# Kernel optimization log

Hardware: AMD Instinct MI355X
Metric: run time of the kernel (lower is better)

## Reference

```python
import jax, jax.numpy as jnp
import numpy as np

N_NODES = 50000
N_EDGES = 800000
D = 96
LN_EPS = 1e-5


def setup_inputs() -> dict:
    key = jax.random.key(0)
    ks = jax.random.split(key, 4)
    x = jax.random.normal(ks[0], (N_NODES, D), dtype=jnp.float32)
    edge_index = jax.random.randint(ks[1], (2, N_EDGES), 0, N_NODES, dtype=jnp.int64)
    scale = 1.0 / np.sqrt(D)
    W0 = jax.random.normal(ks[2], (D, D), dtype=jnp.float32) * scale
    W1 = jax.random.normal(ks[3], (D, D), dtype=jnp.float32) * scale
    b0 = jnp.zeros((D,), jnp.float32)
    b1 = jnp.zeros((D,), jnp.float32)
    g0 = jnp.ones((D,), jnp.float32)
    g1 = jnp.ones((D,), jnp.float32)
    be0 = jnp.zeros((D,), jnp.float32)
    be1 = jnp.zeros((D,), jnp.float32)
    return {"x": x, "edge_index": edge_index, "W0": W0, "b0": b0, "g0": g0,
            "be0": be0, "W1": W1, "b1": b1, "g1": g1, "be1": be1}


def _layer(h, src, dst, norm, n_nodes, W, b, g, be):
    # GCNConv: h' = scatter_add(norm * (h W)[src]) + b  (self-loops included in src/dst)
    h = h @ W                                  # [N, out]
    msg = h[src] * norm[:, None]               # [E+N, out] gather (memory-bound)
    h = jax.ops.segment_sum(msg, dst, num_segments=n_nodes) + b
    h = jnp.tanh(h)
    mu = jnp.mean(h, axis=-1, keepdims=True)
    var = jnp.mean(jnp.square(h - mu), axis=-1, keepdims=True)
    h = (h - mu) * jax.lax.rsqrt(var + LN_EPS)
    return h * g + be


def reference(x, edge_index, W0, b0, g0, be0, W1, b1, g1, be1):
    n = x.shape[0]
    loops = jnp.arange(n, dtype=edge_index.dtype)
    src = jnp.concatenate([edge_index[0], loops])  # add self-loops (PyG default)
    dst = jnp.concatenate([edge_index[1], loops])
    deg = jax.ops.segment_sum(jnp.ones(src.shape, x.dtype), dst, num_segments=n)
    dis = jax.lax.rsqrt(deg)                       # deg >= 1 due to self-loops
    norm = dis[src] * dis[dst]                     # symmetric normalization
    h = _layer(x, src, dst, norm, n, W0, b0, g0, be0)
    h = _layer(h, src, dst, norm, n, W1, b1, g1, be1)
    return h  # dropout is identity in eval mode
```

## Files before the change

kernel.cpp:

```cpp
#include <hip/hip_runtime.h>
#include <hip/hip_bf16.h>
#include <type_traits>

#define D 96
#define LN_EPS 1e-5f
#define CHUNK 1024
#define BCAP 8192
#define BCAPP (BCAP + 1792)

typedef unsigned short ushort_t;
typedef __attribute__((ext_vector_type(8))) short short8;
typedef __attribute__((ext_vector_type(4))) float f32x4;

__device__ __forceinline__ ushort_t f2bf(float f) {
    unsigned u = __float_as_uint(f);
    u += 0x7FFF + ((u >> 16) & 1);
    return (ushort_t)(u >> 16);
}
__device__ __forceinline__ float blo(unsigned v) {
    return __uint_as_float(v << 16);
}
__device__ __forceinline__ float bhi(unsigned v) {
    return __uint_as_float(v & 0xffff0000u);
}

__global__ __launch_bounds__(256) void k_init(const unsigned* __restrict__ w,
                                              int* __restrict__ flag,
                                              int* __restrict__ gcur,
                                              unsigned* __restrict__ hsA,
                                              unsigned* __restrict__ hsB, int N,
                                              int nbuk,
                                              const float* __restrict__ W0,
                                              const float* __restrict__ W1,
                                              ushort_t* __restrict__ Wt0,
                                              ushort_t* __restrict__ Wt1) {
    int t = threadIdx.x;
    if (blockIdx.x == 0) {
        __shared__ int anynz;
        if (t == 0) anynz = 0;
        __syncthreads();
        if ((t & 1) && w[t] != 0) anynz = 1;
        if (t < nbuk) gcur[t] = t * BCAP;
        if (t < 32) hsA[(size_t)N * 32 + t] = 0;
        if (t < 16) hsB[(size_t)N * 16 + t] = 0;
        __syncthreads();
        if (t == 0) *flag = (anynz == 0) ? 1 : 0;
    } else {
        int idx = (blockIdx.x - 1) * 256 + t;
        int sel = idx / 9216, i = idx % 9216;
        int c = i / 96, k = i % 96;
        const float* W = sel ? W1 : W0;
        ushort_t* Wt = sel ? Wt1 : Wt0;
        Wt[c * 96 + k] = f2bf(W[k * 96 + c]);
    }
}

__device__ __forceinline__ int load_idx(const void* eb, int is64, long long pos) {
    if (is64) return (int)((const long long*)eb)[pos];
    return ((const int*)eb)[pos];
}

__global__ __launch_bounds__(256) void k_bfill(const void* __restrict__ eb,
                                               const int* __restrict__ flag,
                                               int* __restrict__ gcur,
                                               unsigned* __restrict__ part, int E) {
    __shared__ int hist[2][256];
    __shared__ int cur[2][256];
    int t = threadIdx.x;
    int half = t >> 7;
    hist[0][t] = 0; hist[1][t] = 0;
    __syncthreads();
    int is64 = *flag;
    long long base = (long long)blockIdx.x * CHUNK;
    int sv[CHUNK / 256];
    int dv[CHUNK / 256];
    #pragma unroll
    for (int i = 0; i < CHUNK / 256; ++i) {
        long long e = base + t + (long long)i * 256;
        if (e < E) {
            sv[i] = load_idx(eb, is64, e);
            dv[i] = load_idx(eb, is64, (long long)E + e);
            atomicAdd(&hist[half][dv[i] >> 8], 1);
        } else dv[i] = -1;
    }
    __syncthreads();
    int h0 = hist[0][t], tot = h0 + hist[1][t];
    int b0 = 0;
    if (tot > 0) b0 = atomicAdd(&gcur[t], tot);
    cur[0][t] = b0;
    cur[1][t] = b0 + h0;
    __syncthreads();
    #pragma unroll
    for (int i = 0; i < CHUNK / 256; ++i) {
        if (dv[i] >= 0) {
            int b = dv[i] >> 8;
            int pos = atomicAdd(&cur[half][b], 1);
            part[pos] = ((unsigned)sv[i] << 8) | (unsigned)(dv[i] & 255);
        }
    }
}

__global__ __launch_bounds__(256) void k_build(const unsigned* __restrict__ part,
                                               const int* __restrict__ gcur,
                                               int2* __restrict__ rr,
                                               int* __restrict__ csr_src,
                                               float* __restrict__ dis,
                                               int N) {
    __shared__ int bins[2][256];
    __shared__ int cur[2][256];
    __shared__ int sh[256];
    int t = threadIdx.x;
    int b = blockIdx.x;
    int half = t >> 7;
    int beg = b * BCAP, end = gcur[b];
    bins[0][t] = 0; bins[1][t] = 0;
    __syncthreads();
    for (int i = beg + t; i < end; i += 256)
        atomicAdd(&bins[half][part[i] & 255u], 1);
    __syncthreads();
    int d0 = bins[0][t];
    int deg = d0 + bins[1][t];
    int pdeg = (deg + 7) & ~7;
    sh[t] = pdeg;
    __syncthreads();
    for (int off = 1; off < 256; off <<= 1) {
        int x = (t >= off) ? sh[t - off] : 0;
        __syncthreads();
        sh[t] += x;
        __syncthreads();
    }
    int mybeg = b * BCAPP + (sh[t] - pdeg);
    int node = b * 256 + t;
    if (node < N) {
        rr[node] = make_int2(mybeg, mybeg + pdeg);
        dis[node] = rsqrtf((float)(deg + 1));
    }
    cur[0][t] = mybeg;
    cur[1][t] = mybeg + d0;
    __syncthreads();
    for (int i = beg + t; i < end; i += 256) {
        unsigned p = part[i];
        int pos = atomicAdd(&cur[half][p & 255u], 1);
        csr_src[pos] = (int)(p >> 8);
    }
    for (int k = deg; k < pdeg; ++k) csr_src[mybeg + k] = N;
}

template<typename T>
__global__ __launch_bounds__(256) void k_gemm_mfma(const T* __restrict__ A0,
                                                   const T* __restrict__ A1,
                                                   const ushort_t* __restrict__ Wt,
                                                   const float* __restrict__ dis,
                                                   ushort_t* __restrict__ HsA,
                                                   ushort_t* __restrict__ HsB, int N) {
    __shared__ ushort_t As[64][104];
    __shared__ ushort_t Bs[96][104];
    int t = threadIdx.x;
    int row0 = blockIdx.x * 64;

    if constexpr (std::is_same<T, float>::value) {
        const float4* X4 = (const float4*)A0;
        #pragma unroll
        for (int i = 0; i < 6; ++i) {
            int idx = t + i * 256;
            int r = idx / 24, c4 = idx % 24;
            float4 v = make_float4(0.f, 0.f, 0.f, 0.f);
            if (row0 + r < N) v = X4[(size_t)(row0 + r) * 24 + c4];
            ushort4 o;
            o.x = f2bf(v.x); o.y = f2bf(v.y); o.z = f2bf(v.z); o.w = f2bf(v.w);
            *(ushort4*)&As[r][c4 * 4] = o;
        }
    } else {
        #pragma unroll
        for (int i = 0; i < 3; ++i) {
            int idx = t + i * 256;
            int r = idx / 12, c8 = idx % 12;
            short8 v = {0, 0, 0, 0, 0, 0, 0, 0};
            if (row0 + r < N) {
                if (c8 < 8) v = *(const short8*)(A0 + (size_t)(row0 + r) * 64 + c8 * 8);
                else        v = *(const short8*)(A1 + (size_t)(row0 + r) * 32 + (c8 - 8) * 8);
            }
            *(short8*)&As[r][c8 * 8] = v;
        }
    }
    #pragma unroll
    for (int i = 0; i < 5; ++i) {
        int idx = t + i * 256;
        if (idx < 1152) {
            int r = idx / 12, c8 = idx % 12;
            *(short8*)&Bs[r][c8 * 8] = *(const short8*)(Wt + r * 96 + c8 * 8);
        }
    }
    __syncthreads();

    int w = t >> 6, l = t & 63;
    int lr = l & 15, lq = l >> 4;
    f32x4 acc[6];
    #pragma unroll
    for (int c = 0; c < 6; ++c) acc[c] = (f32x4){0.f, 0.f, 0.f, 0.f};

    #pragma unroll
    for (int q = 0; q < 3; ++q) {
        short8 af = *(const short8*)&As[w * 16 + lr][q * 32 + lq * 8];
        #pragma unroll
        for (int c = 0; c < 6; ++c) {
            short8 bf = *(const short8*)&Bs[c * 16 + lr][q * 32 + lq * 8];
            acc[c] = __builtin_amdgcn_mfma_f32_16x16x32_bf16(af, bf, acc[c], 0, 0, 0);
        }
    }

    int rbase = row0 + w * 16 + lq * 4;
    #pragma unroll
    for (int r = 0; r < 4; ++r) {
        int gr = rbase + r;
        if (gr < N) {
            float dr = dis[gr];
            ushort_t* oA = HsA + (size_t)gr * 64 + lr;
            ushort_t* oB = HsB + (size_t)gr * 32 + lr;
            #pragma unroll
            for (int c = 0; c < 4; ++c) oA[c * 16] = f2bf(dr * acc[c][r]);
            #pragma unroll
            for (int c = 4; c < 6; ++c) oB[(c - 4) * 16] = f2bf(dr * acc[c][r]);
        }
    }
}

template<bool BF16OUT>
__global__ __launch_bounds__(256) void k_agg_ln(const unsigned* __restrict__ hA32,
                                                const unsigned* __restrict__ hB32,
                                                const int2* __restrict__ rr,
                                                const int* __restrict__ csr_src,
                                                const float* __restrict__ dis,
                                                const float* __restrict__ b,
                                                const float* __restrict__ g,
                                                const float* __restrict__ be,
                                                void* __restrict__ outA,
                                                void* __restrict__ outB, int N) {
    int node = blockIdx.x * 8 + (threadIdx.x >> 5);
    int lane = threadIdx.x & 31;
    if (node >= N) return;

    float a0, a1, c0 = 0.f, c1 = 0.f;
    {
        unsigned v = hA32[(size_t)node * 32 + lane];
        a0 = blo(v); a1 = bhi(v);
        if (lane < 16) {
            unsigned u = hB32[(size_t)node * 16 + lane];
            c0 = blo(u); c1 = bhi(u);
        }
    }

    int2 r = rr[node];
    int beg = r.x, end = r.y;
    int lsel = lane >> 4;
    int lb = lane & 15;
    for (int cb = beg; cb < end; cb += 32) {
        int m = min(32, end - cb);
        int e = cb + lane;
        int sreg = (e < end) ? csr_src[e] : (int)N;
        for (int j = 0; j < m; j += 8) {
            int s0 = __shfl(sreg, j, 32);
            int s1 = __shfl(sreg, j + 1, 32);
            int s2 = __shfl(sreg, j + 2, 32);
            int s3 = __shfl(sreg, j + 3, 32);
            int s4 = __shfl(sreg, j + 4, 32);
            int s5 = __shfl(sreg, j + 5, 32);
            int s6 = __shfl(sreg, j + 6, 32);
            int s7 = __shfl(sreg, j + 7, 32);
            int p0 = __shfl(sreg, j + lsel, 32);
            int p1 = __shfl(sreg, j + 2 + lsel, 32);
            int p2 = __shfl(sreg, j + 4 + lsel, 32);
            int p3 = __shfl(sreg, j + 6 + lsel, 32);
            unsigned v0 = hA32[s0 * 32 + lane];
            unsigned v1 = hA32[s1 * 32 + lane];
            unsigned v2 = hA32[s2 * 32 + lane];
            unsigned v3 = hA32[s3 * 32 + lane];
            unsigned v4 = hA32[s4 * 32 + lane];
            unsigned v5 = hA32[s5 * 32 + lane];
            unsigned v6 = hA32[s6 * 32 + lane];
            unsigned v7 = hA32[s7 * 32 + lane];
            unsigned w0 = hB32[p0 * 16 + lb];
            unsigned w1 = hB32[p1 * 16 + lb];
            unsigned w2 = hB32[p2 * 16 + lb];
            unsigned w3 = hB32[p3 * 16 + lb];
            a0 += blo(v0) + blo(v1) + blo(v2) + blo(v3)
                + blo(v4) + blo(v5) + blo(v6) + blo(v7);
            a1 += bhi(v0) + bhi(v1) + bhi(v2) + bhi(v3)
                + bhi(v4) + bhi(v5) + bhi(v6) + bhi(v7);
            c0 += blo(w0) + blo(w1) + blo(w2) + blo(w3);
            c1 += bhi(w0) + bhi(w1) + bhi(w2) + bhi(w3);
        }
    }

    c0 += __shfl_xor(c0, 16, 32);
    c1 += __shfl_xor(c1, 16, 32);

    float dn = dis[node];
    float2 b01 = ((const float2*)b)[lane];
    a0 = tanhf(fmaf(dn, a0, b01.x));
    a1 = tanhf(fmaf(dn, a1, b01.y));
    float s1 = a0 + a1;
    float s2 = a0 * a0 + a1 * a1;
    float a2 = 0.f, a3 = 0.f;
    if (lane < 16) {
        float2 b23 = ((const float2*)b)[32 + lane];
        a2 = tanhf(fmaf(dn, c0, b23.x));
        a3 = tanhf(fmaf(dn, c1, b23.y));
        s1 += a2 + a3;
        s2 += a2 * a2 + a3 * a3;
    }
    #pragma unroll
    for (int off = 16; off >= 1; off >>= 1) {
        s1 += __shfl_xor(s1, off, 32);
        s2 += __shfl_xor(s2, off, 32);
    }
    float mu = s1 * (1.f / 96.f);
    float var = s2 * (1.f / 96.f) - mu * mu;
    float inv = rsqrtf(var + LN_EPS);

    float2 g01 = ((const float2*)g)[lane];
    float2 e01 = ((const float2*)be)[lane];
    float r0 = (a0 - mu) * inv * g01.x + e01.x;
    float r1 = (a1 - mu) * inv * g01.y + e01.y;
    if (BF16OUT) {
        ((unsigned*)outA)[(size_t)node * 32 + lane] =
            ((unsigned)f2bf(r1) << 16) | (unsigned)f2bf(r0);
        if (lane < 16) {
            float2 g23 = ((const float2*)g)[32 + lane];
            float2 e23 = ((const float2*)be)[32 + lane];
            float r2 = (a2 - mu) * inv * g23.x + e23.x;
            float r3 = (a3 - mu) * inv * g23.y + e23.y;
            ((unsigned*)outB)[(size_t)node * 16 + lane] =
                ((unsigned)f2bf(r3) << 16) | (unsigned)f2bf(r2);
        }
    } else {
        float2* o2 = (float2*)((float*)outA + (size_t)node * D);
        o2[lane] = make_float2(r0, r1);
        if (lane < 16) {
            float2 g23 = ((const float2*)g)[32 + lane];
            float2 e23 = ((const float2*)be)[32 + lane];
            o2[32 + lane] = make_float2((a2 - mu) * inv * g23.x + e23.x,
                                        (a3 - mu) * inv * g23.y + e23.y);
        }
    }
}

extern "C" void kernel_launch(void* const* d_in, const int* in_sizes, int n_in,
                              void* d_out, int out_size, void* d_ws, size_t ws_size,
                              hipStream_t stream) {
    const float* x  = (const float*)d_in[0];
    const void*  eb = d_in[1];
    const float* W0 = (const float*)d_in[2];
    const float* b0 = (const float*)d_in[3];
    const float* g0 = (const float*)d_in[4];
    const float* be0 = (const float*)d_in[5];
    const float* W1 = (const float*)d_in[6];
    const float* b1 = (const float*)d_in[7];
    const float* g1 = (const float*)d_in[8];
    const float* be1 = (const float*)d_in[9];

    const int N = in_sizes[0] / D;
    const int E = in_sizes[1] / 2;
    const int NBUK = (N + 255) >> 8;
    const int NBLK = (E + CHUNK - 1) / CHUNK;

    auto al = [](size_t v) { return (v + 255) & ~(size_t)255; };
    char* w = (char*)d_ws;
    size_t off = 0;
    int* flag = (int*)(w + off);          off = al(off + 4);
    int* gcur = (int*)(w + off);          off = al(off + 256 * 4);
    int2* rr = (int2*)(w + off);          off = al(off + (size_t)N * 8);
    float* dis = (float*)(w + off);       off = al(off + (size_t)N * 4);
    int* csr_src = (int*)(w + off);       off = al(off + ((size_t)NBUK * BCAPP + 64) * 4);
    unsigned* part = (unsigned*)(w + off); off = al(off + ((size_t)NBUK * BCAP + BCAP) * 4);
    unsigned* hsA = (unsigned*)(w + off); off = al(off + ((size_t)N + 1) * 128);
    unsigned* hsB = (unsigned*)(w + off); off = al(off + ((size_t)N + 1) * 64);
    ushort_t* h1A = (ushort_t*)(w + off); off = al(off + (size_t)N * 128);
    ushort_t* h1B = (ushort_t*)(w + off); off = al(off + (size_t)N * 64);
    ushort_t* Wt0 = (ushort_t*)(w + off); off = al(off + 9216 * 2);
    ushort_t* Wt1 = (ushort_t*)(w + off); off = al(off + 9216 * 2);
    float* outf = (float*)d_out;

    const int nbG = (N + 63) / 64;
    const int nbA = (N + 7) / 8;

    k_init<<<73, 256, 0, stream>>>((const unsigned*)eb, flag, gcur, hsA, hsB, N,
                                   NBUK, W0, W1, Wt0, Wt1);
    k_bfill<<<NBLK, 256, 0, stream>>>(eb, flag, gcur, part, E);
    k_build<<<NBUK, 256, 0, stream>>>(part, gcur, rr, csr_src, dis, N);

    k_gemm_mfma<float><<<nbG, 256, 0, stream>>>(x, (const float*)nullptr, Wt0, dis,
                                                (ushort_t*)hsA, (ushort_t*)hsB, N);
    k_agg_ln<true><<<nbA, 256, 0, stream>>>(hsA, hsB, rr, csr_src, dis,
                                            b0, g0, be0, (void*)h1A, (void*)h1B, N);
    k_gemm_mfma<ushort_t><<<nbG, 256, 0, stream>>>(h1A, h1B, Wt1, dis,
                                                   (ushort_t*)hsA, (ushort_t*)hsB, N);
    k_agg_ln<false><<<nbA, 256, 0, stream>>>(hsA, hsB, rr, csr_src, dis,
                                             b1, g1, be1, (void*)outf, nullptr, N);
}
```

Before: 120.4 us.

## Fuse layer-0 GEMM with edge bucketing and relocate degree scaling

The first-layer MFMA GEMM and the edge bucket-fill now run as interleaved block roles of one launch, so the dense work overlaps the atomic-heavy partitioning. Because the GEMM then runs before degrees are known, k_build rescales the projected rows by dis in place. The second layer's dis scaling moves into the layer-1 aggregation output, which is valid because row scaling commutes with the matmul. The weight transpose is folded into each GEMM's shared-memory load, dropping the separate transpose blocks and buffers. The cost is an extra read-modify-write pass over the projected features and a second bf16 rounding of those values.

```diff
diff --git a/kernel.cpp b/kernel.cpp
--- a/kernel.cpp
+++ b/kernel.cpp
@@ -1,6 +1,5 @@
 #include <hip/hip_runtime.h>
 #include <hip/hip_bf16.h>
-#include <type_traits>
 
 #define D 96
 #define LN_EPS 1e-5f
@@ -23,36 +22,26 @@
 __device__ __forceinline__ float bhi(unsigned v) {
     return __uint_as_float(v & 0xffff0000u);
 }
+__device__ __forceinline__ unsigned pack2(float lo, float hi) {
+    return ((unsigned)f2bf(hi) << 16) | (unsigned)f2bf(lo);
+}
 
 __global__ __launch_bounds__(256) void k_init(const unsigned* __restrict__ w,
                                               int* __restrict__ flag,
                                               int* __restrict__ gcur,
                                               unsigned* __restrict__ hsA,
-                                              unsigned* __restrict__ hsB, int N,
-                                              int nbuk,
-                                              const float* __restrict__ W0,
-                                              const float* __restrict__ W1,
-                                              ushort_t* __restrict__ Wt0,
-                                              ushort_t* __restrict__ Wt1) {
+                                              unsigned* __restrict__ hsB,
+                                              int N, int nbuk) {
+    __shared__ int anynz;
     int t = threadIdx.x;
-    if (blockIdx.x == 0) {
-        __shared__ int anynz;
-        if (t == 0) anynz = 0;
-        __syncthreads();
-        if ((t & 1) && w[t] != 0) anynz = 1;
-        if (t < nbuk) gcur[t] = t * BCAP;
-        if (t < 32) hsA[(size_t)N * 32 + t] = 0;
-        if (t < 16) hsB[(size_t)N * 16 + t] = 0;
-        __syncthreads();
-        if (t == 0) *flag = (anynz == 0) ? 1 : 0;
-    } else {
-        int idx = (blockIdx.x - 1) * 256 + t;
-        int sel = idx / 9216, i = idx % 9216;
-        int c = i / 96, k = i % 96;
-        const float* W = sel ? W1 : W0;
-        ushort_t* Wt = sel ? Wt1 : Wt0;
-        Wt[c * 96 + k] = f2bf(W[k * 96 + c]);
-    }
+    if (t == 0) anynz = 0;
+    __syncthreads();
+    if ((t & 1) && w[t] != 0) anynz = 1;
+    if (t < nbuk) gcur[t] = t * BCAP;
+    if (t < 32) hsA[(size_t)N * 32 + t] = 0;
+    if (t < 16) hsB[(size_t)N * 16 + t] = 0;
+    __syncthreads();
+    if (t == 0) *flag = (anynz == 0) ? 1 : 0;
 }
 
 __device__ __forceinline__ int load_idx(const void* eb, int is64, long long pos) {
@@ -60,42 +49,117 @@
     return ((const int*)eb)[pos];
 }
 
-__global__ __launch_bounds__(256) void k_bfill(const void* __restrict__ eb,
-                                               const int* __restrict__ flag,
-                                               int* __restrict__ gcur,
-                                               unsigned* __restrict__ part, int E) {
-    __shared__ int hist[2][256];
-    __shared__ int cur[2][256];
+union Smem1 {
+    struct { ushort_t As[64][104]; ushort_t Bs[96][104]; } g;
+    struct { int hist[2][256]; int cur[2][256]; } b;
+};
+
+__global__ __launch_bounds__(256) void k_fused1(const float* __restrict__ X,
+                                                const float* __restrict__ W0,
+                                                ushort_t* __restrict__ HsA,
+                                                ushort_t* __restrict__ HsB,
+                                                int N, int nbG,
+                                                const void* __restrict__ eb,
+                                                const int* __restrict__ flag,
+                                                int* __restrict__ gcur,
+                                                unsigned* __restrict__ part, int E,
+                                                int NBLK) {
+    __shared__ Smem1 u;
     int t = threadIdx.x;
-    int half = t >> 7;
-    hist[0][t] = 0; hist[1][t] = 0;
-    __syncthreads();
-    int is64 = *flag;
-    long long base = (long long)blockIdx.x * CHUNK;
-    int sv[CHUNK / 256];
-    int dv[CHUNK / 256];
-    #pragma unroll
-    for (int i = 0; i < CHUNK / 256; ++i) {
-        long long e = base + t + (long long)i * 256;
-        if (e < E) {
-            sv[i] = load_idx(eb, is64, e);
-            dv[i] = load_idx(eb, is64, (long long)E + e);
-            atomicAdd(&hist[half][dv[i] >> 8], 1);
-        } else dv[i] = -1;
-    }
-    __syncthreads();
-    int h0 = hist[0][t], tot = h0 + hist[1][t];
-    int b0 = 0;
-    if (tot > 0) b0 = atomicAdd(&gcur[t], tot);
-    cur[0][t] = b0;
-    cur[1][t] = b0 + h0;
-    __syncthreads();
-    #pragma unroll
-    for (int i = 0; i < CHUNK / 256; ++i) {
-        if (dv[i] >= 0) {
-            int b = dv[i] >> 8;
-            int pos = atomicAdd(&cur[half][b], 1);
-            part[pos] = ((unsigned)sv[i] << 8) | (unsigned)(dv[i] & 255);
+    int bid = blockIdx.x;
+    int mn = min(nbG, NBLK);
+    int isG, idx;
+    if (bid < 2 * mn) { isG = !(bid & 1); idx = bid >> 1; }
+    else {
+        int r = bid - 2 * mn;
+        if (nbG > NBLK) { isG = 1; idx = mn + r; }
+        else            { isG = 0; idx = mn + r; }
+    }
+
+    if (isG) {
+        int row0 = idx * 64;
+        const float4* X4 = (const float4*)X;
+        #pragma unroll
+        for (int i = 0; i < 6; ++i) {
+            int id2 = t + i * 256;
+            int r = id2 / 24, c4 = id2 % 24;
+            float4 v = make_float4(0.f, 0.f, 0.f, 0.f);
+            if (row0 + r < N) v = X4[(size_t)(row0 + r) * 24 + c4];
+            ushort4 o;
+            o.x = f2bf(v.x); o.y = f2bf(v.y); o.z = f2bf(v.z); o.w = f2bf(v.w);
+            *(ushort4*)&u.g.As[r][c4 * 4] = o;
+        }
+        const float4* W4 = (const float4*)W0;
+        #pragma unroll
+        for (int i = 0; i < 9; ++i) {
+            int id2 = t + i * 256;
+            int k = id2 / 24, c4 = id2 % 24;
+            float4 v = W4[id2];
+            u.g.Bs[c4 * 4 + 0][k] = f2bf(v.x);
+            u.g.Bs[c4 * 4 + 1][k] = f2bf(v.y);
+            u.g.Bs[c4 * 4 + 2][k] = f2bf(v.z);
+            u.g.Bs[c4 * 4 + 3][k] = f2bf(v.w);
+        }
+        __syncthreads();
+
+        int w = t >> 6, l = t & 63;
+        int lr = l & 15, lq = l >> 4;
+        f32x4 acc[6];
+        #pragma unroll
+        for (int c = 0; c < 6; ++c) acc[c] = (f32x4){0.f, 0.f, 0.f, 0.f};
+        #pragma unroll
+        for (int q = 0; q < 3; ++q) {
+            short8 af = *(const short8*)&u.g.As[w * 16 + lr][q * 32 + lq * 8];
+            #pragma unroll
+            for (int c = 0; c < 6; ++c) {
+                short8 bf = *(const short8*)&u.g.Bs[c * 16 + lr][q * 32 + lq * 8];
+                acc[c] = __builtin_amdgcn_mfma_f32_16x16x32_bf16(af, bf, acc[c], 0, 0, 0);
+            }
+        }
+        int rbase = row0 + w * 16 + lq * 4;
+        #pragma unroll
+        for (int r = 0; r < 4; ++r) {
+            int gr = rbase + r;
+            if (gr < N) {
+                ushort_t* oA = HsA + (size_t)gr * 64 + lr;
+                ushort_t* oB = HsB + (size_t)gr * 32 + lr;
+                #pragma unroll
+                for (int c = 0; c < 4; ++c) oA[c * 16] = f2bf(acc[c][r]);
+                #pragma unroll
+                for (int c = 4; c < 6; ++c) oB[(c - 4) * 16] = f2bf(acc[c][r]);
+            }
+        }
+    } else {
+        int half = t >> 7;
+        u.b.hist[0][t] = 0; u.b.hist[1][t] = 0;
+        __syncthreads();
+        int is64 = *flag;
+        long long base = (long long)idx * CHUNK;
+        int sv[CHUNK / 256];
+        int dv[CHUNK / 256];
+        #pragma unroll
+        for (int i = 0; i < CHUNK / 256; ++i) {
+            long long e = base + t + (long long)i * 256;
+            if (e < E) {
+                sv[i] = load_idx(eb, is64, e);
+                dv[i] = load_idx(eb, is64, (long long)E + e);
+                atomicAdd(&u.b.hist[half][dv[i] >> 8], 1);
+            } else dv[i] = -1;
+        }
+        __syncthreads();
+        int h0 = u.b.hist[0][t], tot = h0 + u.b.hist[1][t];
+        int b0 = 0;
+        if (tot > 0) b0 = atomicAdd(&gcur[t], tot);
+        u.b.cur[0][t] = b0;
+        u.b.cur[1][t] = b0 + h0;
+        __syncthreads();
+        #pragma unroll
+        for (int i = 0; i < CHUNK / 256; ++i) {
+            if (dv[i] >= 0) {
+                int b = dv[i] >> 8;
+                int pos = atomicAdd(&u.b.cur[half][b], 1);
+                part[pos] = ((unsigned)sv[i] << 8) | (unsigned)(dv[i] & 255);
+            }
         }
     }
 }
@@ -105,10 +169,13 @@
                                                int2* __restrict__ rr,
                                                int* __restrict__ csr_src,
                                                float* __restrict__ dis,
+                                               unsigned* __restrict__ hsA,
+                                               unsigned* __restrict__ hsB,
                                                int N) {
     __shared__ int bins[2][256];
     __shared__ int cur[2][256];
     __shared__ int sh[256];
+    __shared__ float disl[256];
     int t = threadIdx.x;
     int b = blockIdx.x;
     int half = t >> 7;
@@ -131,9 +198,11 @@
     }
     int mybeg = b * BCAPP + (sh[t] - pdeg);
     int node = b * 256 + t;
+    float dv = rsqrtf((float)(deg + 1));
+    disl[t] = dv;
     if (node < N) {
         rr[node] = make_int2(mybeg, mybeg + pdeg);
-        dis[node] = rsqrtf((float)(deg + 1));
+        dis[node] = dv;
     }
     cur[0][t] = mybeg;
     cur[1][t] = mybeg + d0;
@@ -144,52 +213,61 @@
         csr_src[pos] = (int)(p >> 8);
     }
     for (int k = deg; k < pdeg; ++k) csr_src[mybeg + k] = N;
-}
-
-template<typename T>
-__global__ __launch_bounds__(256) void k_gemm_mfma(const T* __restrict__ A0,
-                                                   const T* __restrict__ A1,
-                                                   const ushort_t* __restrict__ Wt,
-                                                   const float* __restrict__ dis,
-                                                   ushort_t* __restrict__ HsA,
-                                                   ushort_t* __restrict__ HsB, int N) {
+    __syncthreads();
+    int base = b * 256;
+    #pragma unroll 4
+    for (int i = t; i < 256 * 32; i += 256) {
+        int nd = base + (i >> 5);
+        if (nd < N) {
+            float dn = disl[i >> 5];
+            size_t p = (size_t)nd * 32 + (i & 31);
+            unsigned v = hsA[p];
+            hsA[p] = pack2(blo(v) * dn, bhi(v) * dn);
+        }
+    }
+    #pragma unroll 4
+    for (int i = t; i < 256 * 16; i += 256) {
+        int nd = base + (i >> 4);
+        if (nd < N) {
+            float dn = disl[i >> 4];
+            size_t p = (size_t)nd * 16 + (i & 15);
+            unsigned v = hsB[p];
+            hsB[p] = pack2(blo(v) * dn, bhi(v) * dn);
+        }
+    }
+}
+
+__global__ __launch_bounds__(256) void k_gemm2(const ushort_t* __restrict__ A0,
+                                               const ushort_t* __restrict__ A1,
+                                               const float* __restrict__ W1,
+                                               ushort_t* __restrict__ HsA,
+                                               ushort_t* __restrict__ HsB, int N) {
     __shared__ ushort_t As[64][104];
     __shared__ ushort_t Bs[96][104];
     int t = threadIdx.x;
     int row0 = blockIdx.x * 64;
 
-    if constexpr (std::is_same<T, float>::value) {
-        const float4* X4 = (const float4*)A0;
-        #pragma unroll
-        for (int i = 0; i < 6; ++i) {
-            int idx = t + i * 256;
-            int r = idx / 24, c4 = idx % 24;
-            float4 v = make_float4(0.f, 0.f, 0.f, 0.f);
-            if (row0 + r < N) v = X4[(size_t)(row0 + r) * 24 + c4];
-            ushort4 o;
-            o.x = f2bf(v.x); o.y = f2bf(v.y); o.z = f2bf(v.z); o.w = f2bf(v.w);
-            *(ushort4*)&As[r][c4 * 4] = o;
-        }
-    } else {
-        #pragma unroll
-        for (int i = 0; i < 3; ++i) {
-            int idx = t + i * 256;
-            int r = idx / 12, c8 = idx % 12;
-            short8 v = {0, 0, 0, 0, 0, 0, 0, 0};
-            if (row0 + r < N) {
-                if (c8 < 8) v = *(const short8*)(A0 + (size_t)(row0 + r) * 64 + c8 * 8);
-                else        v = *(const short8*)(A1 + (size_t)(row0 + r) * 32 + (c8 - 8) * 8);
-            }
-            *(short8*)&As[r][c8 * 8] = v;
-        }
-    }
-    #pragma unroll
-    for (int i = 0; i < 5; ++i) {
+    #pragma unroll
+    for (int i = 0; i < 3; ++i) {
         int idx = t + i * 256;
-        if (idx < 1152) {
-            int r = idx / 12, c8 = idx % 12;
-            *(short8*)&Bs[r][c8 * 8] = *(const short8*)(Wt + r * 96 + c8 * 8);
-        }
+        int r = idx / 12, c8 = idx % 12;
+        short8 v = {0, 0, 0, 0, 0, 0, 0, 0};
+        if (row0 + r < N) {
+            if (c8 < 8) v = *(const short8*)(A0 + (size_t)(row0 + r) * 64 + c8 * 8);
+            else        v = *(const short8*)(A1 + (size_t)(row0 + r) * 32 + (c8 - 8) * 8);
+        }
+        *(short8*)&As[r][c8 * 8] = v;
+    }
+    const float4* W4 = (const float4*)W1;
+    #pragma unroll
+    for (int i = 0; i < 9; ++i) {
+        int idx = t + i * 256;
+        int k = idx / 24, c4 = idx % 24;
+        float4 v = W4[idx];
+        Bs[c4 * 4 + 0][k] = f2bf(v.x);
+        Bs[c4 * 4 + 1][k] = f2bf(v.y);
+        Bs[c4 * 4 + 2][k] = f2bf(v.z);
+        Bs[c4 * 4 + 3][k] = f2bf(v.w);
     }
     __syncthreads();
 
@@ -198,7 +276,6 @@
     f32x4 acc[6];
     #pragma unroll
     for (int c = 0; c < 6; ++c) acc[c] = (f32x4){0.f, 0.f, 0.f, 0.f};
-
     #pragma unroll
     for (int q = 0; q < 3; ++q) {
         short8 af = *(const short8*)&As[w * 16 + lr][q * 32 + lq * 8];
@@ -208,19 +285,17 @@
             acc[c] = __builtin_amdgcn_mfma_f32_16x16x32_bf16(af, bf, acc[c], 0, 0, 0);
         }
     }
-
     int rbase = row0 + w * 16 + lq * 4;
     #pragma unroll
     for (int r = 0; r < 4; ++r) {
         int gr = rbase + r;
         if (gr < N) {
-            float dr = dis[gr];
             ushort_t* oA = HsA + (size_t)gr * 64 + lr;
             ushort_t* oB = HsB + (size_t)gr * 32 + lr;
             #pragma unroll
-            for (int c = 0; c < 4; ++c) oA[c * 16] = f2bf(dr * acc[c][r]);
+            for (int c = 0; c < 4; ++c) oA[c * 16] = f2bf(acc[c][r]);
             #pragma unroll
-            for (int c = 4; c < 6; ++c) oB[(c - 4) * 16] = f2bf(dr * acc[c][r]);
+            for (int c = 4; c < 6; ++c) oB[(c - 4) * 16] = f2bf(acc[c][r]);
         }
     }
 }
@@ -245,8 +320,8 @@
         unsigned v = hA32[(size_t)node * 32 + lane];
         a0 = blo(v); a1 = bhi(v);
         if (lane < 16) {
-            unsigned u = hB32[(size_t)node * 16 + lane];
-            c0 = blo(u); c1 = bhi(u);
+            unsigned uu = hB32[(size_t)node * 16 + lane];
+            c0 = blo(uu); c1 = bhi(uu);
         }
     }
 
@@ -323,15 +398,13 @@
     float r0 = (a0 - mu) * inv * g01.x + e01.x;
     float r1 = (a1 - mu) * inv * g01.y + e01.y;
     if (BF16OUT) {
-        ((unsigned*)outA)[(size_t)node * 32 + lane] =
-            ((unsigned)f2bf(r1) << 16) | (unsigned)f2bf(r0);
+        ((unsigned*)outA)[(size_t)node * 32 + lane] = pack2(r0 * dn, r1 * dn);
         if (lane < 16) {
             float2 g23 = ((const float2*)g)[32 + lane];
             float2 e23 = ((const float2*)be)[32 + lane];
-            float r2 = (a2 - mu) * inv * g23.x + e23.x;
-            float r3 = (a3 - mu) * inv * g23.y + e23.y;
-            ((unsigned*)outB)[(size_t)node * 16 + lane] =
-                ((unsigned)f2bf(r3) << 16) | (unsigned)f2bf(r2);
+            float r2 = ((a2 - mu) * inv * g23.x + e23.x) * dn;
+            float r3 = ((a3 - mu) * inv * g23.y + e23.y) * dn;
+            ((unsigned*)outB)[(size_t)node * 16 + lane] = pack2(r2, r3);
         }
     } else {
         float2* o2 = (float2*)((float*)outA + (size_t)node * D);
@@ -375,26 +448,21 @@
     unsigned* part = (unsigned*)(w + off); off = al(off + ((size_t)NBUK * BCAP + BCAP) * 4);
     unsigned* hsA = (unsigned*)(w + off); off = al(off + ((size_t)N + 1) * 128);
     unsigned* hsB = (unsigned*)(w + off); off = al(off + ((size_t)N + 1) * 64);
-    ushort_t* h1A = (ushort_t*)(w + off); off = al(off + (size_t)N * 128);
-    ushort_t* h1B = (ushort_t*)(w + off); off = al(off + (size_t)N * 64);
-    ushort_t* Wt0 = (ushort_t*)(w + off); off = al(off + 9216 * 2);
-    ushort_t* Wt1 = (ushort_t*)(w + off); off = al(off + 9216 * 2);
+    unsigned* h1A = (unsigned*)(w + off); off = al(off + (size_t)N * 128);
+    unsigned* h1B = (unsigned*)(w + off); off = al(off + (size_t)N * 64);
     float* outf = (float*)d_out;
 
     const int nbG = (N + 63) / 64;
     const int nbA = (N + 7) / 8;
 
-    k_init<<<73, 256, 0, stream>>>((const unsigned*)eb, flag, gcur, hsA, hsB, N,
-                                   NBUK, W0, W1, Wt0, Wt1);
-    k_bfill<<<NBLK, 256, 0, stream>>>(eb, flag, gcur, part, E);
-    k_build<<<NBUK, 256, 0, stream>>>(part, gcur, rr, csr_src, dis, N);
-
-    k_gemm_mfma<float><<<nbG, 256, 0, stream>>>(x, (const float*)nullptr, Wt0, dis,
-                                                (ushort_t*)hsA, (ushort_t*)hsB, N);
+    k_init<<<1, 256, 0, stream>>>((const unsigned*)eb, flag, gcur, hsA, hsB, N, NBUK);
+    k_fused1<<<nbG + NBLK, 256, 0, stream>>>(x, W0, (ushort_t*)hsA, (ushort_t*)hsB,
+                                             N, nbG, eb, flag, gcur, part, E, NBLK);
+    k_build<<<NBUK, 256, 0, stream>>>(part, gcur, rr, csr_src, dis, hsA, hsB, N);
     k_agg_ln<true><<<nbA, 256, 0, stream>>>(hsA, hsB, rr, csr_src, dis,
                                             b0, g0, be0, (void*)h1A, (void*)h1B, N);
-    k_gemm_mfma<ushort_t><<<nbG, 256, 0, stream>>>(h1A, h1B, Wt1, dis,
-                                                   (ushort_t*)hsA, (ushort_t*)hsB, N);
+    k_gemm2<<<nbG, 256, 0, stream>>>((const ushort_t*)h1A, (const ushort_t*)h1B, W1,
+                                     (ushort_t*)hsA, (ushort_t*)hsB, N);
     k_agg_ln<false><<<nbA, 256, 0, stream>>>(hsA, hsB, rr, csr_src, dis,
                                              b1, g1, be1, (void*)outf, nullptr, N);
 }
```

New measurement: 131.2 us. 9.0% more time.

## Coalesce bucket fill via shared-memory sort and fold weight transpose into GEMM

Applied to the files above, without the earlier changes.

The edge bucket-fill kernel now sorts each chunk's packed edges by bucket in shared memory, using a prefix scan, and then writes them to the global partition array in contiguous runs instead of scattering them with per-edge atomics. Each bfill block now detects the index dtype itself, so the separate flag buffer goes away. The weight transpose and bf16 conversion moves into the GEMM kernel, which loads fp32 W and transposes it into shared memory, so the init kernel shrinks to one block. The aim is better write coalescing and a lighter init kernel, at the cost of every GEMM block redoing the weight conversion and extra shared memory and barriers in bfill.

```diff
diff --git a/kernel.cpp b/kernel.cpp
--- a/kernel.cpp
+++ b/kernel.cpp
@@ -24,53 +24,135 @@
     return __uint_as_float(v & 0xffff0000u);
 }
 
-__global__ __launch_bounds__(256) void k_init(const unsigned* __restrict__ w,
-                                              int* __restrict__ flag,
-                                              int* __restrict__ gcur,
-                                              unsigned* __restrict__ hsA,
-                                              unsigned* __restrict__ hsB, int N,
-                                              int nbuk,
-                                              const float* __restrict__ W0,
-                                              const float* __restrict__ W1,
-                                              ushort_t* __restrict__ Wt0,
-                                              ushort_t* __restrict__ Wt1) {
-    int t = threadIdx.x;
-    if (blockIdx.x == 0) {
-        __shared__ int anynz;
-        if (t == 0) anynz = 0;
-        __syncthreads();
-        if ((t & 1) && w[t] != 0) anynz = 1;
-        if (t < nbuk) gcur[t] = t * BCAP;
-        if (t < 32) hsA[(size_t)N * 32 + t] = 0;
-        if (t < 16) hsB[(size_t)N * 16 + t] = 0;
-        __syncthreads();
-        if (t == 0) *flag = (anynz == 0) ? 1 : 0;
-    } else {
-        int idx = (blockIdx.x - 1) * 256 + t;
-        int sel = idx / 9216, i = idx % 9216;
-        int c = i / 96, k = i % 96;
-        const float* W = sel ? W1 : W0;
-        ushort_t* Wt = sel ? Wt1 : Wt0;
-        Wt[c * 96 + k] = f2bf(W[k * 96 + c]);
-    }
-}
-
 __device__ __forceinline__ int load_idx(const void* eb, int is64, long long pos) {
     if (is64) return (int)((const long long*)eb)[pos];
     return ((const int*)eb)[pos];
 }
 
+template<typename T, bool INIT>
+__global__ __launch_bounds__(256) void k_gemm_mfma(const T* __restrict__ A0,
+                                                   const T* __restrict__ A1,
+                                                   const float* __restrict__ W,
+                                                   const float* __restrict__ dis,
+                                                   ushort_t* __restrict__ HsA,
+                                                   ushort_t* __restrict__ HsB, int N,
+                                                   int* __restrict__ gcur, int nbuk) {
+    __shared__ ushort_t As[64][104];
+    __shared__ ushort_t Bs[96][104];
+    int t = threadIdx.x;
+    int row0 = blockIdx.x * 64;
+
+    if constexpr (INIT) {
+        if (blockIdx.x == 0) {
+            if (t < nbuk) gcur[t] = t * BCAP;
+            if (t < 32) ((unsigned*)HsA)[(size_t)N * 32 + t] = 0;
+            if (t < 16) ((unsigned*)HsB)[(size_t)N * 16 + t] = 0;
+        }
+    }
+
+    if constexpr (std::is_same<T, float>::value) {
+        const float4* X4 = (const float4*)A0;
+        #pragma unroll
+        for (int i = 0; i < 6; ++i) {
+            int idx = t + i * 256;
+            int r = idx / 24, c4 = idx % 24;
+            float4 v = make_float4(0.f, 0.f, 0.f, 0.f);
+            if (row0 + r < N) v = X4[(size_t)(row0 + r) * 24 + c4];
+            ushort4 o;
+            o.x = f2bf(v.x); o.y = f2bf(v.y); o.z = f2bf(v.z); o.w = f2bf(v.w);
+            *(ushort4*)&As[r][c4 * 4] = o;
+        }
+    } else {
+        #pragma unroll
+        for (int i = 0; i < 3; ++i) {
+            int idx = t + i * 256;
+            int r = idx / 12, c8 = idx % 12;
+            short8 v = {0, 0, 0, 0, 0, 0, 0, 0};
+            if (row0 + r < N) {
+                if (c8 < 8) v = *(const short8*)(A0 + (size_t)(row0 + r) * 64 + c8 * 8);
+                else        v = *(const short8*)(A1 + (size_t)(row0 + r) * 32 + (c8 - 8) * 8);
+            }
+            *(short8*)&As[r][c8 * 8] = v;
+        }
+    }
+    const float4* W4 = (const float4*)W;
+    #pragma unroll
+    for (int i = 0; i < 9; ++i) {
+        int idx = t + i * 256;
+        int k = idx / 24, c4 = idx % 24;
+        float4 v = W4[idx];
+        Bs[c4 * 4 + 0][k] = f2bf(v.x);
+        Bs[c4 * 4 + 1][k] = f2bf(v.y);
+        Bs[c4 * 4 + 2][k] = f2bf(v.z);
+        Bs[c4 * 4 + 3][k] = f2bf(v.w);
+    }
+    __syncthreads();
+
+    int w = t >> 6, l = t & 63;
+    int lr = l & 15, lq = l >> 4;
+    f32x4 acc[6];
+    #pragma unroll
+    for (int c = 0; c < 6; ++c) acc[c] = (f32x4){0.f, 0.f, 0.f, 0.f};
+
+    #pragma unroll
+    for (int q = 0; q < 3; ++q) {
+        short8 af = *(const short8*)&As[w * 16 + lr][q * 32 + lq * 8];
+        #pragma unroll
+        for (int c = 0; c < 6; ++c) {
+            short8 bf = *(const short8*)&Bs[c * 16 + lr][q * 32 + lq * 8];
+            acc[c] = __builtin_amdgcn_mfma_f32_16x16x32_bf16(af, bf, acc[c], 0, 0, 0);
+        }
+    }
+
+    int rbase = row0 + w * 16 + lq * 4;
+    #pragma unroll
+    for (int r = 0; r < 4; ++r) {
+        int gr = rbase + r;
+        if (gr < N) {
+            float dr = dis[gr];
+            ushort_t* oA = HsA + (size_t)gr * 64 + lr;
+            ushort_t* oB = HsB + (size_t)gr * 32 + lr;
+            #pragma unroll
+            for (int c = 0; c < 4; ++c) oA[c * 16] = f2bf(dr * acc[c][r]);
+            #pragma unroll
+            for (int c = 4; c < 6; ++c) oB[(c - 4) * 16] = f2bf(dr * acc[c][r]);
+        }
+    }
+}
+
+
+__global__ __launch_bounds__(256) void k_init(int* __restrict__ gcur,
+                                              unsigned* __restrict__ hsA,
+                                              unsigned* __restrict__ hsB,
+                                              int N, int nbuk) {
+    int t = threadIdx.x;
+    if (t < nbuk) gcur[t] = t * BCAP;
+    if (t < 32) hsA[(size_t)N * 32 + t] = 0;
+    if (t < 16) hsB[(size_t)N * 16 + t] = 0;
+}
+
 __global__ __launch_bounds__(256) void k_bfill(const void* __restrict__ eb,
-                                               const int* __restrict__ flag,
                                                int* __restrict__ gcur,
                                                unsigned* __restrict__ part, int E) {
     __shared__ int hist[2][256];
-    __shared__ int cur[2][256];
+    __shared__ int lcur[2][256];
+    __shared__ int sh[256];
+    __shared__ int loc[256];
+    __shared__ int gbase[256];
+    __shared__ unsigned sorted[CHUNK];
+    __shared__ unsigned char bkt[CHUNK];
+    __shared__ int anynz;
+    __shared__ int totsum;
     int t = threadIdx.x;
     int half = t >> 7;
+
+    if (t == 0) anynz = 0;
     hist[0][t] = 0; hist[1][t] = 0;
     __syncthreads();
-    int is64 = *flag;
+    if ((t & 1) && ((const unsigned*)eb)[t] != 0) anynz = 1;
+    __syncthreads();
+    int is64 = (anynz == 0) ? 1 : 0;
+
     long long base = (long long)blockIdx.x * CHUNK;
     int sv[CHUNK / 256];
     int dv[CHUNK / 256];
@@ -85,18 +167,37 @@
     }
     __syncthreads();
     int h0 = hist[0][t], tot = h0 + hist[1][t];
-    int b0 = 0;
-    if (tot > 0) b0 = atomicAdd(&gcur[t], tot);
-    cur[0][t] = b0;
-    cur[1][t] = b0 + h0;
+    int gb = 0;
+    if (tot > 0) gb = atomicAdd(&gcur[t], tot);
+    gbase[t] = gb;
+    sh[t] = tot;
+    __syncthreads();
+    for (int off = 1; off < 256; off <<= 1) {
+        int x = (t >= off) ? sh[t - off] : 0;
+        __syncthreads();
+        sh[t] += x;
+        __syncthreads();
+    }
+    int excl = sh[t] - tot;
+    loc[t] = excl;
+    lcur[0][t] = excl;
+    lcur[1][t] = excl + h0;
+    if (t == 255) totsum = sh[255];
     __syncthreads();
     #pragma unroll
     for (int i = 0; i < CHUNK / 256; ++i) {
         if (dv[i] >= 0) {
-            int b = dv[i] >> 8;
-            int pos = atomicAdd(&cur[half][b], 1);
-            part[pos] = ((unsigned)sv[i] << 8) | (unsigned)(dv[i] & 255);
-        }
+            int bk = dv[i] >> 8;
+            int pos = atomicAdd(&lcur[half][bk], 1);
+            sorted[pos] = ((unsigned)sv[i] << 8) | (unsigned)(dv[i] & 255);
+            bkt[pos] = (unsigned char)bk;
+        }
+    }
+    __syncthreads();
+    int tts = totsum;
+    for (int i = t; i < tts; i += 256) {
+        int bk = bkt[i];
+        part[gbase[bk] + (i - loc[bk])] = sorted[i];
     }
 }
 
@@ -146,85 +247,6 @@
     for (int k = deg; k < pdeg; ++k) csr_src[mybeg + k] = N;
 }
 
-template<typename T>
-__global__ __launch_bounds__(256) void k_gemm_mfma(const T* __restrict__ A0,
-                                                   const T* __restrict__ A1,
-                                                   const ushort_t* __restrict__ Wt,
-                                                   const float* __restrict__ dis,
-                                                   ushort_t* __restrict__ HsA,
-                                                   ushort_t* __restrict__ HsB, int N) {
-    __shared__ ushort_t As[64][104];
-    __shared__ ushort_t Bs[96][104];
-    int t = threadIdx.x;
-    int row0 = blockIdx.x * 64;
-
-    if constexpr (std::is_same<T, float>::value) {
-        const float4* X4 = (const float4*)A0;
-        #pragma unroll
-        for (int i = 0; i < 6; ++i) {
-            int idx = t + i * 256;
-            int r = idx / 24, c4 = idx % 24;
-            float4 v = make_float4(0.f, 0.f, 0.f, 0.f);
-            if (row0 + r < N) v = X4[(size_t)(row0 + r) * 24 + c4];
-            ushort4 o;
-            o.x = f2bf(v.x); o.y = f2bf(v.y); o.z = f2bf(v.z); o.w = f2bf(v.w);
-            *(ushort4*)&As[r][c4 * 4] = o;
-        }
-    } else {
-        #pragma unroll
-        for (int i = 0; i < 3; ++i) {
-            int idx = t + i * 256;
-            int r = idx / 12, c8 = idx % 12;
-            short8 v = {0, 0, 0, 0, 0, 0, 0, 0};
-            if (row0 + r < N) {
-                if (c8 < 8) v = *(const short8*)(A0 + (size_t)(row0 + r) * 64 + c8 * 8);
-                else        v = *(const short8*)(A1 + (size_t)(row0 + r) * 32 + (c8 - 8) * 8);
-            }
-            *(short8*)&As[r][c8 * 8] = v;
-        }
-    }
-    #pragma unroll
-    for (int i = 0; i < 5; ++i) {
-        int idx = t + i * 256;
-        if (idx < 1152) {
-            int r = idx / 12, c8 = idx % 12;
-            *(short8*)&Bs[r][c8 * 8] = *(const short8*)(Wt + r * 96 + c8 * 8);
-        }
-    }
-    __syncthreads();
-
-    int w = t >> 6, l = t & 63;
-    int lr = l & 15, lq = l >> 4;
-    f32x4 acc[6];
-    #pragma unroll
-    for (int c = 0; c < 6; ++c) acc[c] = (f32x4){0.f, 0.f, 0.f, 0.f};
-
-    #pragma unroll
-    for (int q = 0; q < 3; ++q) {
-        short8 af = *(const short8*)&As[w * 16 + lr][q * 32 + lq * 8];
-        #pragma unroll
-        for (int c = 0; c < 6; ++c) {
-            short8 bf = *(const short8*)&Bs[c * 16 + lr][q * 32 + lq * 8];
-            acc[c] = __builtin_amdgcn_mfma_f32_16x16x32_bf16(af, bf, acc[c], 0, 0, 0);
-        }
-    }
-
-    int rbase = row0 + w * 16 + lq * 4;
-    #pragma unroll
-    for (int r = 0; r < 4; ++r) {
-        int gr = rbase + r;
-        if (gr < N) {
-            float dr = dis[gr];
-            ushort_t* oA = HsA + (size_t)gr * 64 + lr;
-            ushort_t* oB = HsB + (size_t)gr * 32 + lr;
-            #pragma unroll
-            for (int c = 0; c < 4; ++c) oA[c * 16] = f2bf(dr * acc[c][r]);
-            #pragma unroll
-            for (int c = 4; c < 6; ++c) oB[(c - 4) * 16] = f2bf(dr * acc[c][r]);
-        }
-    }
-}
-
 template<bool BF16OUT>
 __global__ __launch_bounds__(256) void k_agg_ln(const unsigned* __restrict__ hA32,
                                                 const unsigned* __restrict__ hB32,
@@ -245,8 +267,8 @@
         unsigned v = hA32[(size_t)node * 32 + lane];
         a0 = blo(v); a1 = bhi(v);
         if (lane < 16) {
-            unsigned u = hB32[(size_t)node * 16 + lane];
-            c0 = blo(u); c1 = bhi(u);
+            unsigned uu = hB32[(size_t)node * 16 + lane];
+            c0 = blo(uu); c1 = bhi(uu);
         }
     }
 
@@ -367,7 +389,6 @@
     auto al = [](size_t v) { return (v + 255) & ~(size_t)255; };
     char* w = (char*)d_ws;
     size_t off = 0;
-    int* flag = (int*)(w + off);          off = al(off + 4);
     int* gcur = (int*)(w + off);          off = al(off + 256 * 4);
     int2* rr = (int2*)(w + off);          off = al(off + (size_t)N * 8);
     float* dis = (float*)(w + off);       off = al(off + (size_t)N * 4);
@@ -375,26 +396,26 @@
     unsigned* part = (unsigned*)(w + off); off = al(off + ((size_t)NBUK * BCAP + BCAP) * 4);
     unsigned* hsA = (unsigned*)(w + off); off = al(off + ((size_t)N + 1) * 128);
     unsigned* hsB = (unsigned*)(w + off); off = al(off + ((size_t)N + 1) * 64);
-    ushort_t* h1A = (ushort_t*)(w + off); off = al(off + (size_t)N * 128);
-    ushort_t* h1B = (ushort_t*)(w + off); off = al(off + (size_t)N * 64);
-    ushort_t* Wt0 = (ushort_t*)(w + off); off = al(off + 9216 * 2);
-    ushort_t* Wt1 = (ushort_t*)(w + off); off = al(off + 9216 * 2);
+    unsigned* h1A = (unsigned*)(w + off); off = al(off + (size_t)N * 128);
+    unsigned* h1B = (unsigned*)(w + off); off = al(off + (size_t)N * 64);
     float* outf = (float*)d_out;
 
     const int nbG = (N + 63) / 64;
     const int nbA = (N + 7) / 8;
 
-    k_init<<<73, 256, 0, stream>>>((const unsigned*)eb, flag, gcur, hsA, hsB, N,
-                                   NBUK, W0, W1, Wt0, Wt1);
-    k_bfill<<<NBLK, 256, 0, stream>>>(eb, flag, gcur, part, E);
+    k_init<<<1, 256, 0, stream>>>(gcur, hsA, hsB, N, NBUK);
+    k_bfill<<<NBLK, 256, 0, stream>>>(eb, gcur, part, E);
     k_build<<<NBUK, 256, 0, stream>>>(part, gcur, rr, csr_src, dis, N);
 
-    k_gemm_mfma<float><<<nbG, 256, 0, stream>>>(x, (const float*)nullptr, Wt0, dis,
-                                                (ushort_t*)hsA, (ushort_t*)hsB, N);
+    k_gemm_mfma<float, false><<<nbG, 256, 0, stream>>>(x, (const float*)nullptr, W0,
+                                                       dis, (ushort_t*)hsA,
+                                                       (ushort_t*)hsB, N, nullptr, 0);
     k_agg_ln<true><<<nbA, 256, 0, stream>>>(hsA, hsB, rr, csr_src, dis,
                                             b0, g0, be0, (void*)h1A, (void*)h1B, N);
-    k_gemm_mfma<ushort_t><<<nbG, 256, 0, stream>>>(h1A, h1B, Wt1, dis,
-                                                   (ushort_t*)hsA, (ushort_t*)hsB, N);
+    k_gemm_mfma<ushort_t, false><<<nbG, 256, 0, stream>>>((const ushort_t*)h1A,
+                                                          (const ushort_t*)h1B, W1,
+                                                          dis, (ushort_t*)hsA,
+                                                          (ushort_t*)hsB, N, nullptr, 0);
     k_agg_ln<false><<<nbA, 256, 0, stream>>>(hsA, hsB, rr, csr_src, dis,
                                              b1, g1, be1, (void*)outf, nullptr, N);
 }
```

Result: slower. 126.9 us (+5.4%).
